# Optimization experiments

Measured on AMD Instinct MI355X. Metric: run time of the kernel, lower is better.

## Reference

```python
import jax, jax.numpy as jnp
import numpy as np

T, B, I, H = 256, 32, 128, 256
CLIP = 2.0

def setup_inputs() -> dict:
    key = jax.random.key(0)
    ks = jax.random.split(key, 10)
    si, sh = 1.0 / np.sqrt(I), 1.0 / np.sqrt(H)
    return {
        "x":     jax.random.normal(ks[0], (T, B, I), jnp.float32),
        "Wx":    jax.random.normal(ks[1], (4 * H, I), jnp.float32) * si,
        "bx":    jax.random.normal(ks[2], (4 * H,), jnp.float32) * si,
        "Wh":    jax.random.normal(ks[3], (4 * H, H), jnp.float32) * sh,
        "bh":    jax.random.normal(ks[4], (4 * H,), jnp.float32) * sh,
        "w_mod": jax.random.normal(ks[5], (1, H), jnp.float32) * sh,
        "b_mod": jax.random.normal(ks[6], (1,), jnp.float32) * sh,
        "w_fan": jax.random.normal(ks[7], (H, 1), jnp.float32),
        "b_fan": jax.random.normal(ks[8], (H,), jnp.float32),
        "alpha": 1e-4 * jax.random.uniform(ks[9], (H, H), jnp.float32),
    }

def reference(x, Wx, bx, Wh, bh, w_mod, b_mod, w_fan, b_fan, alpha):
    Bn = x.shape[1]
    # precompute input projection for all timesteps: [T, B, 4H]
    xf = jnp.einsum('tbi,gi->tbg', x, Wx) + bx

    def step(state, xf_t):
        h, c, hebb = state  # h,c: [B,H]; hebb: [B,H,H]
        fioj = xf_t + h @ Wh.T + bh                     # [B,4H]
        f = jax.nn.sigmoid(fioj[:, :H])
        i = jax.nn.sigmoid(fioj[:, H:2 * H])
        o = jax.nn.sigmoid(fioj[:, 2 * H:3 * H])
        # h_pred @ (alpha * hebb) : batched vec-mat product
        plast = jnp.einsum('bh,hk,bhk->bk', h, alpha, hebb)
        j = jnp.tanh(fioj[:, 3 * H:] + plast)
        c_new = f * c + i * j
        h_new = o * jnp.tanh(c_new)
        eta = jnp.tanh(c_new @ w_mod.T + b_mod)          # [B,1]
        myeta = eta * w_fan[:, 0] + b_fan                # [B,H] (Linear(1,H) fanout)
        # delta_hebb = outer(h_pred, j); eta modulates along the j axis
        hebb_new = jnp.clip(hebb + myeta[:, None, :] * (h[:, :, None] * j[:, None, :]),
                            -CLIP, CLIP)
        return (h_new, c_new, hebb_new), h_new

    init = (jnp.zeros((Bn, H), jnp.float32),
            jnp.zeros((Bn, H), jnp.float32),
            jnp.zeros((Bn, H, H), jnp.float32))
    (h, c, hebb), hs = jax.lax.scan(step, init, xf)
    return hs, h, c, hebb
```

## Files before the change

### kernel.cpp

```cpp
#include <hip/hip_runtime.h>


#define TT 256
#define BB 32
#define II 128
#define HH 256
#define G4 1024

typedef _Float16 h2_t __attribute__((ext_vector_type(2)));
typedef unsigned long long u64;

__device__ __forceinline__ float sigm(float x) {
    return 1.0f / (1.0f + __expf(-x));
}
__device__ __forceinline__ float tanhfast(float x) {
    return 1.0f - 2.0f / (__expf(2.0f * x) + 1.0f);
}
__device__ __forceinline__ unsigned pkh(float lo, float hi) {
    h2_t v;
    v.x = (_Float16)lo;
    v.y = (_Float16)hi;
    return __builtin_bit_cast(unsigned, v);
}

#if __has_builtin(__builtin_amdgcn_fdot2)
__device__ __forceinline__ float dot2(unsigned a, unsigned b, float c) {
    return __builtin_amdgcn_fdot2(__builtin_bit_cast(h2_t, a),
                                  __builtin_bit_cast(h2_t, b), c, false);
}
#else
__device__ __forceinline__ float dot2(unsigned a, unsigned b, float c) {
    h2_t av = __builtin_bit_cast(h2_t, a), bv = __builtin_bit_cast(h2_t, b);
    return c + (float)av.x * (float)bv.x + (float)av.y * (float)bv.y;
}
#endif

__device__ __forceinline__ h2_t pkfma(h2_t a, h2_t b, h2_t c) {
#if __has_builtin(__builtin_elementwise_fma)
    return __builtin_elementwise_fma(a, b, c);
#else
    return a * b + c;
#endif
}
__device__ __forceinline__ h2_t clip2h(h2_t x) {
    const h2_t lo = {(_Float16)-2.0f, (_Float16)-2.0f};
    const h2_t hi = {(_Float16)2.0f, (_Float16)2.0f};
#if __has_builtin(__builtin_elementwise_max) && __has_builtin(__builtin_elementwise_min)
    return __builtin_elementwise_min(__builtin_elementwise_max(x, lo), hi);
#else
    h2_t r = x;
    r.x = r.x < lo.x ? lo.x : (r.x > hi.x ? hi.x : r.x);
    r.y = r.y < lo.y ? lo.y : (r.y > hi.y ? hi.y : r.y);
    return r;
#endif
}

__global__ __launch_bounds__(256) void prep_wd3(const float* __restrict__ Wh,
                                                uint4* __restrict__ Wd3) {
    int idx = blockIdx.x * 256 + threadIdx.x;
    int ro = idx >> 12, rem = idx & 4095;
    int g = rem >> 2, ri = rem & 3;
    int r8 = 4 * ro + ri;
    const float4* s = (const float4*)(Wh + (size_t)g * HH + (r8 << 3));
    float4 a = s[0], b2 = s[1];
    uint4 o;
    o.x = pkh(a.x, a.y);
    o.y = pkh(a.z, a.w);
    o.z = pkh(b2.x, b2.y);
    o.w = pkh(b2.z, b2.w);
    Wd3[idx] = o;
}

__global__ __launch_bounds__(256) void prep_alq(const float* __restrict__ alpha,
                                                uint4* __restrict__ alQ) {
    int idx = blockIdx.x * 256 + threadIdx.x;
    int p4 = idx >> 8, k = idx & 255;
    unsigned r[4];
#pragma unroll
    for (int j = 0; j < 4; ++j) {
        int p = 4 * p4 + j;
        float a0 = alpha[(size_t)(2 * p) * HH + k];
        float a1 = alpha[(size_t)(2 * p + 1) * HH + k];
        r[j] = pkh(a0, a1);
    }
    uint4 o; o.x = r[0]; o.y = r[1]; o.z = r[2]; o.w = r[3];
    alQ[idx] = o;
}

__global__ __launch_bounds__(256) void xf_gemm(const float* __restrict__ x,
                                               const float* __restrict__ Wx,
                                               const float* __restrict__ bx,
                                               const float* __restrict__ bh,
                                               float* __restrict__ xf) {
    __shared__ float As[64][37];
    __shared__ float Bs[64][37];
    const int tid = threadIdx.x;
    const int tx = tid & 15, ty = tid >> 4;
    const int m0 = blockIdx.y << 6;
    const int n0 = blockIdx.x << 6;
    float c[4][4] = {};

    for (int k0 = 0; k0 < II; k0 += 32) {
#pragma unroll
        for (int hh = 0; hh < 2; ++hh) {
            int row = (tid >> 3) + (hh << 5);
            int col = (tid & 7) << 2;
            float4 va = *(const float4*)(x + (size_t)(m0 + row) * II + k0 + col);
            As[row][col] = va.x; As[row][col + 1] = va.y;
            As[row][col + 2] = va.z; As[row][col + 3] = va.w;
            float4 vb = *(const float4*)(Wx + (size_t)(n0 + row) * II + k0 + col);
            Bs[row][col] = vb.x; Bs[row][col + 1] = vb.y;
            Bs[row][col + 2] = vb.z; Bs[row][col + 3] = vb.w;
        }
        __syncthreads();
#pragma unroll
        for (int kk = 0; kk < 32; ++kk) {
            float a[4], bb[4];
#pragma unroll
            for (int u = 0; u < 4; ++u) a[u] = As[(ty << 2) + u][kk];
#pragma unroll
            for (int v = 0; v < 4; ++v) bb[v] = Bs[(tx << 2) + v][kk];
#pragma unroll
            for (int u = 0; u < 4; ++u)
#pragma unroll
                for (int v = 0; v < 4; ++v)
                    c[u][v] = fmaf(a[u], bb[v], c[u][v]);
        }
        __syncthreads();
    }
    const int n = n0 + (tx << 2);
    float4 bxv = *(const float4*)(bx + n);
    float4 bhv = *(const float4*)(bh + n);
    float4 badd = {bxv.x + bhv.x, bxv.y + bhv.y, bxv.z + bhv.z, bxv.w + bhv.w};
#pragma unroll
    for (int u = 0; u < 4; ++u) {
        int m = m0 + (ty << 2) + u;
        float4 o = {c[u][0] + badd.x, c[u][1] + badd.y,
                    c[u][2] + badd.z, c[u][3] + badd.w};
        *(float4*)(xf + (size_t)m * G4 + n) = o;
    }
}

#define HBQ_FOREACH(X) X(0) X(1) X(2) X(3) X(4) X(5) X(6) X(7)

#define HBQ_DECL(i) h2_t hp##i = {(_Float16)0.0f, (_Float16)0.0f};
#define HBQ_OUT(i) \
    hbout[(size_t)(r0g + 2 * i) * HH + k]     = (float)hp##i.x; \
    hbout[(size_t)(r0g + 2 * i + 1) * HH + k] = (float)hp##i.y;

#define HBQ_STEP(i, au, hou, hnu) { \
    h2_t al2 = __builtin_bit_cast(h2_t, au); \
    h2_t ho2 = __builtin_bit_cast(h2_t, hou); \
    h2_t hn2 = __builtin_bit_cast(h2_t, hnu); \
    hp##i = clip2h(pkfma(mj2, ho2, hp##i)); \
    h2_t hna = hn2 * al2; \
    pp = dot2(__builtin_bit_cast(unsigned, hna), \
              __builtin_bit_cast(unsigned, hp##i), pp); }

#define HBQ_CHUNK(q, AV, i0, i1, i2, i3) { \
    uint4 ho = hfO4[hb4 + (q)]; \
    uint4 hn = hfN4[hb4 + (q)]; \
    HBQ_STEP(i0, AV.x, ho.x, hn.x) \
    HBQ_STEP(i1, AV.y, ho.y, hn.y) \
    HBQ_STEP(i2, AV.z, ho.z, hn.z) \
    HBQ_STEP(i3, AV.w, ho.w, hn.w) }

#define HBV_STEP(i, hou) { \
    h2_t ho2 = __builtin_bit_cast(h2_t, hou); \
    hp##i = clip2h(pkfma(mj2, ho2, hp##i)); }
#define HBV_CHUNK(q, i0, i1, i2, i3) { \
    uint4 ho = hfO4[hb4 + (q)]; \
    HBV_STEP(i0, ho.x) HBV_STEP(i1, ho.y) \
    HBV_STEP(i2, ho.z) HBV_STEP(i3, ho.w) }

#define DOTW(W, HV) { \
    ac0 = dot2(W.x, HV.x, ac0); ac1 = dot2(W.y, HV.y, ac1); \
    ac2 = dot2(W.z, HV.z, ac2); ac3 = dot2(W.w, HV.w, ac3); }

__global__ __launch_bounds__(1024, 1) void scan_kernel(
    const float* __restrict__ xf,
    const uint4* __restrict__ Wd3,
    const uint4* __restrict__ alQ,
    const float* __restrict__ w_mod,
    const float* __restrict__ b_mod,
    const float* __restrict__ w_fan,
    const float* __restrict__ b_fan,
    u64* __restrict__ exData,
    float* __restrict__ out) {
    const int bid = blockIdx.x;
    const int r   = bid >> 5;
    const int b   = bid & 31;
    const int tid = threadIdx.x;
    const int k   = tid & (HH - 1);
    const int rg  = tid >> 8;
    const int r0g = r * 64 + rg * 16;
    const int hb4 = r0g >> 3;

    __shared__ alignas(16) unsigned short hf_s[2][HH];
    __shared__ float fioj_s[G4];
    __shared__ float pp_s[4][HH];
    __shared__ float red_s[4];

    HBQ_FOREACH(HBQ_DECL)

    if (tid < HH) {
        hf_s[0][tid] = 0;
        hf_s[1][tid] = 0;
    }
    if (tid < 4) red_s[tid] = 0.0f;
    __syncthreads();

    const float bmod = b_mod[0];
    const float wf = w_fan[k], bf = b_fan[k], wm = w_mod[k];
    float creg = 0.0f, jreg = 0.0f, hnreg = 0.0f;

    const uint4* wb = Wd3 + ((size_t)(2 * r) << 12) + (tid << 2);
    uint4 w0 = wb[0], w1 = wb[1], w2 = wb[2], w3 = wb[3];
    uint4 w4 = wb[4096], w5 = wb[4097], w6 = wb[4098], w7 = wb[4099];
    uint4 aqA = alQ[(size_t)(8 * r + 2 * rg) * 256 + k];
    uint4 aqB = alQ[(size_t)(8 * r + 2 * rg + 1) * 256 + k];

    const float* xfp = xf + (size_t)b * G4 + tid;

    u64* myEx = exData + (size_t)((b * 4 + r) * 2) * 1024;
    const u64* pEx1 = exData + (size_t)((b * 4 + ((r + 1) & 3)) * 2) * 1024;
    const u64* pEx2 = exData + (size_t)((b * 4 + ((r + 2) & 3)) * 2) * 1024;
    const u64* pEx3 = exData + (size_t)((b * 4 + ((r + 3) & 3)) * 2) * 1024;

    for (int t = 0; t < TT; ++t) {
        float xfv = 0.0f;
        if (rg == r) xfv = xfp[(size_t)t * BB * G4];

        float eta = tanhfast(((red_s[0] + red_s[1]) + (red_s[2] + red_s[3])) + bmod);
        float mj = fmaf(eta, wf, bf) * jreg;
        h2_t mj2;
        mj2.x = (_Float16)mj;
        mj2.y = mj2.x;
        const uint4* hfO4 = (const uint4*)hf_s[t & 1];
        const uint4* hfN4 = (const uint4*)hf_s[(t & 1) ^ 1];
        float pp = 0.0f;
        HBQ_CHUNK(0, aqA, 0, 1, 2, 3)
        HBQ_CHUNK(1, aqB, 4, 5, 6, 7)
        pp_s[rg][k] = pp;

        float ac0 = 0.f, ac1 = 0.f, ac2 = 0.f, ac3 = 0.f;
        {
            const int hx = r << 3;
            uint4 h0 = hfN4[hx], h1 = hfN4[hx + 1];
            uint4 h2 = hfN4[hx + 2], h3 = hfN4[hx + 3];
            DOTW(w0, h0) DOTW(w1, h1) DOTW(w2, h2) DOTW(w3, h3)
            uint4 h4 = hfN4[hx + 4], h5 = hfN4[hx + 5];
            uint4 h6 = hfN4[hx + 6], h7 = hfN4[hx + 7];
            DOTW(w4, h4) DOTW(w5, h5) DOTW(w6, h6) DOTW(w7, h7)
        }
        float part = ((ac0 + ac1) + (ac2 + ac3)) + xfv;
        __syncthreads();

        if (tid >= 768) {
            int k2 = tid - 768;
            part += (pp_s[0][k2] + pp_s[1][k2]) + (pp_s[2][k2] + pp_s[3][k2]);
        }

        const unsigned tag = (unsigned)(t + 1);
        const int off = (t & 1) * 1024 + tid;
        {
            u64 pkv = ((u64)tag << 32) |
                      (u64)__builtin_bit_cast(unsigned, part);
            __hip_atomic_store(&myEx[off], pkv, __ATOMIC_RELAXED,
                               __HIP_MEMORY_SCOPE_AGENT);
        }

        {
            float s1 = 0.f, s2 = 0.f, s3 = 0.f;
            bool d1 = false, d2 = false, d3 = false;
            do {
                if (!d1) {
                    u64 v = __hip_atomic_load(&pEx1[off], __ATOMIC_RELAXED,
                                              __HIP_MEMORY_SCOPE_AGENT);
                    if ((unsigned)(v >> 32) == tag) {
                        s1 = __builtin_bit_cast(float, (unsigned)v);
                        d1 = true;
                    }
                }
                if (!d2) {
                    u64 v = __hip_atomic_load(&pEx2[off], __ATOMIC_RELAXED,
                                              __HIP_MEMORY_SCOPE_AGENT);
                    if ((unsigned)(v >> 32) == tag) {
                        s2 = __builtin_bit_cast(float, (unsigned)v);
                        d2 = true;
                    }
                }
                if (!d3) {
                    u64 v = __hip_atomic_load(&pEx3[off], __ATOMIC_RELAXED,
                                              __HIP_MEMORY_SCOPE_AGENT);
                    if ((unsigned)(v >> 32) == tag) {
                        s3 = __builtin_bit_cast(float, (unsigned)v);
                        d3 = true;
                    }
                }
            } while (!(d1 && d2 && d3));
            fioj_s[tid] = part + ((s1 + s2) + s3);
        }
        __syncthreads();

        float fg = sigm(fioj_s[k]);
        float ig = sigm(fioj_s[HH + k]);
        float og = sigm(fioj_s[2 * HH + k]);
        float jp = fioj_s[3 * HH + k];
        jreg = tanhfast(jp);
        creg = fmaf(fg, creg, ig * jreg);
        hnreg = og * tanhfast(creg);
        if (rg == 0) {
            _Float16 hh = (_Float16)hnreg;
            hf_s[t & 1][k] = __builtin_bit_cast(unsigned short, hh);
            if (r == 0) out[((size_t)t * BB + b) * HH + k] = hnreg;
            float e = creg * wm;
#pragma unroll
            for (int m = 32; m >= 1; m >>= 1) e += __shfl_xor(e, m, 64);
            if ((k & 63) == 0) red_s[k >> 6] = e;
        }
        __syncthreads();
    }

    {
        float eta = tanhfast(((red_s[0] + red_s[1]) + (red_s[2] + red_s[3])) + bmod);
        float mj = fmaf(eta, wf, bf) * jreg;
        h2_t mj2;
        mj2.x = (_Float16)mj;
        mj2.y = mj2.x;
        const uint4* hfO4 = (const uint4*)hf_s[0];
        HBV_CHUNK(0, 0, 1, 2, 3)
        HBV_CHUNK(1, 4, 5, 6, 7)
    }

    const size_t HS = (size_t)TT * BB * HH;
    if (r == 0 && rg == 0) {
        out[HS + (size_t)b * HH + k]           = hnreg;
        out[HS + BB * HH + (size_t)b * HH + k] = creg;
    }
    float* hbout = out + HS + 2 * BB * HH + (size_t)b * HH * HH;
    HBQ_FOREACH(HBQ_OUT)
}

extern "C" void kernel_launch(void* const* d_in, const int* in_sizes, int n_in,
                              void* d_out, int out_size, void* d_ws,
                              size_t ws_size, hipStream_t stream) {
    const float* x     = (const float*)d_in[0];
    const float* Wx    = (const float*)d_in[1];
    const float* bx    = (const float*)d_in[2];
    const float* Wh    = (const float*)d_in[3];
    const float* bh    = (const float*)d_in[4];
    const float* w_mod = (const float*)d_in[5];
    const float* b_mod = (const float*)d_in[6];
    const float* w_fan = (const float*)d_in[7];
    const float* b_fan = (const float*)d_in[8];
    const float* alpha = (const float*)d_in[9];
    float* out = (float*)d_out;

    float* xf  = (float*)d_ws;
    uint4* Wd3 = (uint4*)((char*)d_ws + 33554432);
    uint4* alQ = (uint4*)((char*)d_ws + 34078720);
    u64*   exD = (u64*)((char*)d_ws + 34209792);

    hipLaunchKernelGGL(prep_wd3, dim3(128), dim3(256), 0, stream, Wh, Wd3);
    hipLaunchKernelGGL(prep_alq, dim3(32), dim3(256), 0, stream, alpha, alQ);
    hipLaunchKernelGGL(xf_gemm, dim3(16, 128), dim3(256), 0, stream,
                       x, Wx, bx, bh, xf);
    hipLaunchKernelGGL(scan_kernel, dim3(128), dim3(1024), 0, stream,
                       xf, Wd3, alQ, w_mod, b_mod, w_fan, b_fan,
                       exD, out);
}
```

Baseline: 906.7 us.

## Split each batch's recurrence across eight blocks instead of four

The scan kernel now launches 256 blocks, eight per batch element. Each block owns a 32-row slice of the hidden state, which halves its Wh dot-product and Hebbian register work per step. Partial gate sums are exchanged through global memory with seven peers instead of three. Blocks handling the first 768 gate outputs now publish their partials before the block barrier rather than after it. The trade is less compute per block against more cross-block polling traffic and a larger exchange buffer every timestep.

```diff
diff --git a/kernel.cpp b/kernel.cpp
--- a/kernel.cpp
+++ b/kernel.cpp
@@ -141,7 +141,7 @@
     }
 }
 
-#define HBQ_FOREACH(X) X(0) X(1) X(2) X(3) X(4) X(5) X(6) X(7)
+#define HBQ_FOREACH(X) X(0) X(1) X(2) X(3)
 
 #define HBQ_DECL(i) h2_t hp##i = {(_Float16)0.0f, (_Float16)0.0f};
 #define HBQ_OUT(i) \
@@ -157,25 +157,23 @@
     pp = dot2(__builtin_bit_cast(unsigned, hna), \
               __builtin_bit_cast(unsigned, hp##i), pp); }
 
-#define HBQ_CHUNK(q, AV, i0, i1, i2, i3) { \
-    uint4 ho = hfO4[hb4 + (q)]; \
-    uint4 hn = hfN4[hb4 + (q)]; \
-    HBQ_STEP(i0, AV.x, ho.x, hn.x) \
-    HBQ_STEP(i1, AV.y, ho.y, hn.y) \
-    HBQ_STEP(i2, AV.z, ho.z, hn.z) \
-    HBQ_STEP(i3, AV.w, ho.w, hn.w) }
-
 #define HBV_STEP(i, hou) { \
     h2_t ho2 = __builtin_bit_cast(h2_t, hou); \
     hp##i = clip2h(pkfma(mj2, ho2, hp##i)); }
-#define HBV_CHUNK(q, i0, i1, i2, i3) { \
-    uint4 ho = hfO4[hb4 + (q)]; \
-    HBV_STEP(i0, ho.x) HBV_STEP(i1, ho.y) \
-    HBV_STEP(i2, ho.z) HBV_STEP(i3, ho.w) }
 
 #define DOTW(W, HV) { \
     ac0 = dot2(W.x, HV.x, ac0); ac1 = dot2(W.y, HV.y, ac1); \
     ac2 = dot2(W.z, HV.z, ac2); ac3 = dot2(W.w, HV.w, ac3); }
+
+#define POLL_ONE(d, s, P) \
+    if (!d) { \
+        u64 v = __hip_atomic_load(&P[off], __ATOMIC_RELAXED, \
+                                  __HIP_MEMORY_SCOPE_AGENT); \
+        if ((unsigned)(v >> 32) == tag) { \
+            s = __builtin_bit_cast(float, (unsigned)v); \
+            d = true; \
+        } \
+    }
 
 __global__ __launch_bounds__(1024, 1) void scan_kernel(
     const float* __restrict__ xf,
@@ -193,8 +191,8 @@
     const int tid = threadIdx.x;
     const int k   = tid & (HH - 1);
     const int rg  = tid >> 8;
-    const int r0g = r * 64 + rg * 16;
-    const int hb4 = r0g >> 3;
+    const int r0g = r * 32 + rg * 8;
+    const int hb4 = 4 * r + rg;
 
     __shared__ alignas(16) unsigned short hf_s[2][HH];
     __shared__ float fioj_s[G4];
@@ -214,56 +212,66 @@
     const float wf = w_fan[k], bf = b_fan[k], wm = w_mod[k];
     float creg = 0.0f, jreg = 0.0f, hnreg = 0.0f;
 
-    const uint4* wb = Wd3 + ((size_t)(2 * r) << 12) + (tid << 2);
+    const uint4* wb = Wd3 + ((size_t)r << 12) + (tid << 2);
     uint4 w0 = wb[0], w1 = wb[1], w2 = wb[2], w3 = wb[3];
-    uint4 w4 = wb[4096], w5 = wb[4097], w6 = wb[4098], w7 = wb[4099];
-    uint4 aqA = alQ[(size_t)(8 * r + 2 * rg) * 256 + k];
-    uint4 aqB = alQ[(size_t)(8 * r + 2 * rg + 1) * 256 + k];
+    uint4 aq = alQ[(size_t)(4 * r + rg) * 256 + k];
 
     const float* xfp = xf + (size_t)b * G4 + tid;
 
-    u64* myEx = exData + (size_t)((b * 4 + r) * 2) * 1024;
-    const u64* pEx1 = exData + (size_t)((b * 4 + ((r + 1) & 3)) * 2) * 1024;
-    const u64* pEx2 = exData + (size_t)((b * 4 + ((r + 2) & 3)) * 2) * 1024;
-    const u64* pEx3 = exData + (size_t)((b * 4 + ((r + 3) & 3)) * 2) * 1024;
+    u64* myEx = exData + (size_t)((b * 8 + r) * 2) * 1024;
+    const u64* pEx1 = exData + (size_t)((b * 8 + ((r + 1) & 7)) * 2) * 1024;
+    const u64* pEx2 = exData + (size_t)((b * 8 + ((r + 2) & 7)) * 2) * 1024;
+    const u64* pEx3 = exData + (size_t)((b * 8 + ((r + 3) & 7)) * 2) * 1024;
+    const u64* pEx4 = exData + (size_t)((b * 8 + ((r + 4) & 7)) * 2) * 1024;
+    const u64* pEx5 = exData + (size_t)((b * 8 + ((r + 5) & 7)) * 2) * 1024;
+    const u64* pEx6 = exData + (size_t)((b * 8 + ((r + 6) & 7)) * 2) * 1024;
+    const u64* pEx7 = exData + (size_t)((b * 8 + ((r + 7) & 7)) * 2) * 1024;
 
     for (int t = 0; t < TT; ++t) {
+        const unsigned tag = (unsigned)(t + 1);
+        const int off = (t & 1) * 1024 + tid;
+        const uint4* hfO4 = (const uint4*)hf_s[t & 1];
+        const uint4* hfN4 = (const uint4*)hf_s[(t & 1) ^ 1];
+
         float xfv = 0.0f;
-        if (rg == r) xfv = xfp[(size_t)t * BB * G4];
+        if ((tid >> 7) == r) xfv = xfp[(size_t)t * BB * G4];
+
+        float ac0 = 0.f, ac1 = 0.f, ac2 = 0.f, ac3 = 0.f;
+        {
+            const int hx = r << 2;
+            uint4 h0 = hfN4[hx], h1 = hfN4[hx + 1];
+            uint4 h2 = hfN4[hx + 2], h3 = hfN4[hx + 3];
+            DOTW(w0, h0) DOTW(w1, h1) DOTW(w2, h2) DOTW(w3, h3)
+        }
+        float part = ((ac0 + ac1) + (ac2 + ac3)) + xfv;
+
+        if (tid < 768) {
+            u64 pkv = ((u64)tag << 32) |
+                      (u64)__builtin_bit_cast(unsigned, part);
+            __hip_atomic_store(&myEx[off], pkv, __ATOMIC_RELAXED,
+                               __HIP_MEMORY_SCOPE_AGENT);
+        }
 
         float eta = tanhfast(((red_s[0] + red_s[1]) + (red_s[2] + red_s[3])) + bmod);
         float mj = fmaf(eta, wf, bf) * jreg;
         h2_t mj2;
         mj2.x = (_Float16)mj;
         mj2.y = mj2.x;
-        const uint4* hfO4 = (const uint4*)hf_s[t & 1];
-        const uint4* hfN4 = (const uint4*)hf_s[(t & 1) ^ 1];
         float pp = 0.0f;
-        HBQ_CHUNK(0, aqA, 0, 1, 2, 3)
-        HBQ_CHUNK(1, aqB, 4, 5, 6, 7)
+        {
+            uint4 ho = hfO4[hb4];
+            uint4 hn = hfN4[hb4];
+            HBQ_STEP(0, aq.x, ho.x, hn.x)
+            HBQ_STEP(1, aq.y, ho.y, hn.y)
+            HBQ_STEP(2, aq.z, ho.z, hn.z)
+            HBQ_STEP(3, aq.w, ho.w, hn.w)
+        }
         pp_s[rg][k] = pp;
-
-        float ac0 = 0.f, ac1 = 0.f, ac2 = 0.f, ac3 = 0.f;
-        {
-            const int hx = r << 3;
-            uint4 h0 = hfN4[hx], h1 = hfN4[hx + 1];
-            uint4 h2 = hfN4[hx + 2], h3 = hfN4[hx + 3];
-            DOTW(w0, h0) DOTW(w1, h1) DOTW(w2, h2) DOTW(w3, h3)
-            uint4 h4 = hfN4[hx + 4], h5 = hfN4[hx + 5];
-            uint4 h6 = hfN4[hx + 6], h7 = hfN4[hx + 7];
-            DOTW(w4, h4) DOTW(w5, h5) DOTW(w6, h6) DOTW(w7, h7)
-        }
-        float part = ((ac0 + ac1) + (ac2 + ac3)) + xfv;
         __syncthreads();
 
         if (tid >= 768) {
             int k2 = tid - 768;
             part += (pp_s[0][k2] + pp_s[1][k2]) + (pp_s[2][k2] + pp_s[3][k2]);
-        }
-
-        const unsigned tag = (unsigned)(t + 1);
-        const int off = (t & 1) * 1024 + tid;
-        {
             u64 pkv = ((u64)tag << 32) |
                       (u64)__builtin_bit_cast(unsigned, part);
             __hip_atomic_store(&myEx[off], pkv, __ATOMIC_RELAXED,
@@ -271,35 +279,20 @@
         }
 
         {
-            float s1 = 0.f, s2 = 0.f, s3 = 0.f;
-            bool d1 = false, d2 = false, d3 = false;
+            float s1 = 0.f, s2 = 0.f, s3 = 0.f, s4 = 0.f,
+                  s5 = 0.f, s6 = 0.f, s7 = 0.f;
+            bool d1 = false, d2 = false, d3 = false, d4 = false,
+                 d5 = false, d6 = false, d7 = false;
             do {
-                if (!d1) {
-                    u64 v = __hip_atomic_load(&pEx1[off], __ATOMIC_RELAXED,
-                                              __HIP_MEMORY_SCOPE_AGENT);
-                    if ((unsigned)(v >> 32) == tag) {
-                        s1 = __builtin_bit_cast(float, (unsigned)v);
-                        d1 = true;
-                    }
-                }
-                if (!d2) {
-                    u64 v = __hip_atomic_load(&pEx2[off], __ATOMIC_RELAXED,
-                                              __HIP_MEMORY_SCOPE_AGENT);
-                    if ((unsigned)(v >> 32) == tag) {
-                        s2 = __builtin_bit_cast(float, (unsigned)v);
-                        d2 = true;
-                    }
-                }
-                if (!d3) {
-                    u64 v = __hip_atomic_load(&pEx3[off], __ATOMIC_RELAXED,
-                                              __HIP_MEMORY_SCOPE_AGENT);
-                    if ((unsigned)(v >> 32) == tag) {
-                        s3 = __builtin_bit_cast(float, (unsigned)v);
-                        d3 = true;
-                    }
-                }
-            } while (!(d1 && d2 && d3));
-            fioj_s[tid] = part + ((s1 + s2) + s3);
+                POLL_ONE(d1, s1, pEx1)
+                POLL_ONE(d2, s2, pEx2)
+                POLL_ONE(d3, s3, pEx3)
+                POLL_ONE(d4, s4, pEx4)
+                POLL_ONE(d5, s5, pEx5)
+                POLL_ONE(d6, s6, pEx6)
+                POLL_ONE(d7, s7, pEx7)
+            } while (!(d1 && d2 && d3 && d4 && d5 && d6 && d7));
+            fioj_s[tid] = part + (((s1 + s2) + (s3 + s4)) + ((s5 + s6) + s7));
         }
         __syncthreads();
 
@@ -329,8 +322,9 @@
         mj2.x = (_Float16)mj;
         mj2.y = mj2.x;
         const uint4* hfO4 = (const uint4*)hf_s[0];
-        HBV_CHUNK(0, 0, 1, 2, 3)
-        HBV_CHUNK(1, 4, 5, 6, 7)
+        uint4 ho = hfO4[hb4];
+        HBV_STEP(0, ho.x) HBV_STEP(1, ho.y)
+        HBV_STEP(2, ho.z) HBV_STEP(3, ho.w)
     }
 
     const size_t HS = (size_t)TT * BB * HH;
@@ -366,7 +360,7 @@
     hipLaunchKernelGGL(prep_alq, dim3(32), dim3(256), 0, stream, alpha, alQ);
     hipLaunchKernelGGL(xf_gemm, dim3(16, 128), dim3(256), 0, stream,
                        x, Wx, bx, bh, xf);
-    hipLaunchKernelGGL(scan_kernel, dim3(128), dim3(1024), 0, stream,
+    hipLaunchKernelGGL(scan_kernel, dim3(256), dim3(1024), 0, stream,
                        xf, Wd3, alQ, w_mod, b_mod, w_fan, b_fan,
                        exD, out);
 }
```

Measured after the change: 995.8 us. 9.8% more time.
